# Performance work log

Hardware: AMD Instinct MI355X
Metric: run time of the kernel (lower is better)

The kernel has to match this reference:

```python
import jax, jax.numpy as jnp
import numpy as np

B, S, H = 4, 2048, 1024
NH = 1                     # source code only type-checks with 1 head (see notes)
DH = H // NH               # head dim == hidden size
DT = 32                    # distance_type
LN_EPS = 1e-12


def setup_inputs() -> dict:
    key = jax.random.key(0)
    ks = jax.random.split(key, 12)
    sd = 0.02
    hidden_states = jax.random.normal(ks[0], (B, S, H), dtype=jnp.float32)
    attention_mask = jnp.zeros((B, 1, 1, S), dtype=jnp.float32)
    word_word_relation = jax.random.randint(ks[1], (B, S, S), 0, DT, dtype=jnp.int64)
    dist_emb = sd * jax.random.normal(ks[2], (DT, H), dtype=jnp.float32)
    dist_emb = dist_emb.at[0].set(0.0)  # padding_idx=0
    return {
        "hidden_states": hidden_states,
        "attention_mask": attention_mask,
        "word_word_relation": word_word_relation,
        "Wq": sd * jax.random.normal(ks[3], (H, H), dtype=jnp.float32),
        "bq": jnp.zeros((H,), dtype=jnp.float32),
        "Wk": sd * jax.random.normal(ks[4], (H, H), dtype=jnp.float32),
        "bk": jnp.zeros((H,), dtype=jnp.float32),
        "Wv": sd * jax.random.normal(ks[5], (H, H), dtype=jnp.float32),
        "bv": jnp.zeros((H,), dtype=jnp.float32),
        "dist_emb": dist_emb,
        "Wo": sd * jax.random.normal(ks[6], (H, H), dtype=jnp.float32),
        "bo": jnp.zeros((H,), dtype=jnp.float32),
        "ln_g": jnp.ones((H,), dtype=jnp.float32),
        "ln_b": jnp.zeros((H,), dtype=jnp.float32),
    }


def _split_heads(x):
    # [B,S,H] -> [B,NH,S,DH]
    return x.reshape(B, S, NH, DH).transpose(0, 2, 1, 3)


def reference(hidden_states, attention_mask, word_word_relation, Wq, bq, Wk, bk,
              Wv, bv, dist_emb, Wo, bo, ln_g, ln_b):
    q = _split_heads(hidden_states @ Wq.T + bq)   # [B,NH,S,DH]
    k = _split_heads(hidden_states @ Wk.T + bk)
    v = _split_heads(hidden_states @ Wv.T + bv)

    # raw QK^T scores [B,NH,S,S]
    scores = jnp.einsum('bhqd,bhkd->bhqk', q, k)

    # query . distance_embedding^T : [B,NH,S,DT]
    word_dot_distance = jnp.einsum('bhqd,td->bhqt', q, dist_emb)

    rel = word_word_relation[:, None, :, :]       # [B,1,S,S]
    # gather per-pair distance score along the distance-type axis
    dist_att = jnp.take_along_axis(word_dot_distance, rel, axis=3)  # [B,NH,S,S]
    mask_out = (rel == 1).astype(scores.dtype)    # keep only relation==1 pairs
    dist_att = dist_att * mask_out

    scores = (scores + dist_att) / jnp.sqrt(jnp.asarray(DH, scores.dtype))
    scores = scores + attention_mask              # additive BERT mask
    probs = jax.nn.softmax(scores, axis=-1)       # dropout p=0 -> identity

    ctx = jnp.einsum('bhqk,bhkd->bhqd', probs, v) # [B,NH,S,DH]
    ctx = ctx.transpose(0, 2, 1, 3).reshape(B, S, H)

    # BertSelfOutput: dense -> residual -> LayerNorm
    attn_out = ctx @ Wo.T + bo
    x = attn_out + hidden_states
    mu = jnp.mean(x, axis=-1, keepdims=True)
    var = jnp.mean(jnp.square(x - mu), axis=-1, keepdims=True)
    out = (x - mu) * jax.lax.rsqrt(var + LN_EPS) * ln_g + ln_b
    return out
```

## Files before the change

### kernel.cpp

```cpp
#include <hip/hip_runtime.h>

#define BM 128
#define BN 128
#define BKH 32

typedef __bf16 bf16x8 __attribute__((ext_vector_type(8)));
typedef __bf16 bf16x4 __attribute__((ext_vector_type(4)));
typedef float f32x4 __attribute__((ext_vector_type(4)));
typedef __bf16 bf16_t;

__device__ __forceinline__ void gl_lds16(const void* g, void* l) {
    __builtin_amdgcn_global_load_lds(
        (const __attribute__((address_space(1))) void*)g,
        (__attribute__((address_space(3))) void*)l, 16, 0, 0);
}

__global__ __launch_bounds__(256)
void cvt_all_kernel(const float* __restrict__ hid,
                    const float* __restrict__ w0, const float* __restrict__ w1,
                    const float* __restrict__ w2, const float* __restrict__ w3,
                    bf16_t* __restrict__ hidb, bf16_t* __restrict__ wb)
{
    const int bid = blockIdx.x;
    const float* src;
    bf16_t* dst;
    size_t off;
    if (bid < 8192) {
        src = hid; dst = hidb; off = (size_t)bid * 1024;
    } else {
        const int i = (bid - 8192) >> 10;
        src = (i == 0) ? w0 : (i == 1) ? w1 : (i == 2) ? w2 : w3;
        dst = wb + (size_t)i * 1024 * 1024;
        off = (size_t)((bid - 8192) & 1023) * 1024;
    }
    const size_t idx = off + threadIdx.x * 4;
    const float4 v = *(const float4*)(src + idx);
    bf16x4 o;
    o[0] = (__bf16)v.x; o[1] = (__bf16)v.y;
    o[2] = (__bf16)v.z; o[3] = (__bf16)v.w;
    *(bf16x4*)(dst + idx) = o;
}

template <int MODE, int SWIZ>
__global__ __launch_bounds__(256)
void gemm_bt(const bf16_t* __restrict__ A, const bf16_t* __restrict__ Bw,
             const float* __restrict__ bias, const float* __restrict__ bias2,
             const float* __restrict__ bias3,
             bf16_t* __restrict__ C, bf16_t* __restrict__ C2,
             int M, int N, int K,
             long long sAz, long long sBz, long long sCz,
             const bf16_t* __restrict__ resid,
             int Sdim, int DHdim)
{
    const int bz = blockIdx.z;
    const float* bi = bias;
    if (MODE == 0) {
        Bw += (long long)bz * N * K;
        bi = (bz == 0) ? bias : (bz == 1 ? bias2 : bias3);
        if (bz < 2) C += (long long)bz * sCz;
    } else {
        A += (long long)bz * sAz;
        Bw += (long long)bz * sBz;
        C += (long long)bz * sCz;
    }

    int m0, n0;
    if (SWIZ) {
        const int num_n = N / BN;
        const int pid = blockIdx.x;
        const int group = 8 * num_n;
        const int g = pid / group;
        m0 = (g * 8 + (pid % 8)) * BM;
        n0 = ((pid % group) / 8) * BN;
    } else {
        m0 = blockIdx.y * BM;
        n0 = blockIdx.x * BN;
    }
    const int tid = threadIdx.x;
    const int w = tid >> 6;
    const int lane = tid & 63;
    const int wr = w >> 1;
    const int wc = w & 1;
    const int srow = lane >> 2;
    const int scol = (lane & 3) * 8;
    const int frow = lane & 15;
    const int fk = (lane >> 4) * 8;

    __shared__ bf16_t smem[4 * BM * BKH];
    bf16_t* A0 = smem;
    bf16_t* A1 = smem + BM * BKH;
    bf16_t* B0 = smem + 2 * BM * BKH;
    bf16_t* B1 = smem + 3 * BM * BKH;

    f32x4 acc[4][4];
#pragma unroll
    for (int i = 0; i < 4; ++i)
#pragma unroll
        for (int j = 0; j < 4; ++j) acc[i][j] = (f32x4)0.0f;

    for (int k0 = 0; k0 < K; k0 += 2 * BKH) {
#pragma unroll
        for (int i = 0; i < 2; ++i) {
            const int r = i * 64 + w * 16;
            const bf16_t* ga = A + (size_t)(m0 + r + srow) * K + (k0 + scol);
            const bf16_t* gb = Bw + (size_t)(n0 + r + srow) * K + (k0 + scol);
            gl_lds16(ga,        &A0[r * BKH]);
            gl_lds16(ga + BKH,  &A1[r * BKH]);
            gl_lds16(gb,        &B0[r * BKH]);
            gl_lds16(gb + BKH,  &B1[r * BKH]);
        }
        __syncthreads();
#pragma unroll
        for (int h = 0; h < 2; ++h) {
            const bf16_t* Ah = h ? A1 : A0;
            const bf16_t* Bh = h ? B1 : B0;
            bf16x8 af[4], bfv[4];
#pragma unroll
            for (int t = 0; t < 4; ++t) {
                af[t]  = *(const bf16x8*)&Ah[(wr * 64 + t * 16 + frow) * BKH + fk];
                bfv[t] = *(const bf16x8*)&Bh[(wc * 64 + t * 16 + frow) * BKH + fk];
            }
#pragma unroll
            for (int mt = 0; mt < 4; ++mt)
#pragma unroll
                for (int nt = 0; nt < 4; ++nt)
                    acc[mt][nt] = __builtin_amdgcn_mfma_f32_16x16x32_bf16(
                        af[mt], bfv[nt], acc[mt][nt], 0, 0, 0);
        }
        __syncthreads();
    }

    const int crow = (lane >> 4) * 4;
    const int ccol = lane & 15;

    if (MODE == 0 && bz == 2) {
#pragma unroll
        for (int mt = 0; mt < 4; ++mt) {
            const int mb = m0 + wr * 64 + mt * 16 + crow;
#pragma unroll
            for (int nt = 0; nt < 4; ++nt) {
                const int n = n0 + wc * 64 + nt * 16 + ccol;
                const float bv = bi[n];
                const int b = mb >> 11;
                const int s = mb & 2047;
                union { ushort4 u; bf16_t h[4]; } pk;
#pragma unroll
                for (int r = 0; r < 4; ++r) pk.h[r] = (__bf16)(acc[mt][nt][r] + bv);
                *(ushort4*)&C2[(size_t)b * DHdim * Sdim + (size_t)n * Sdim + s] = pk.u;
            }
        }
        return;
    }

    bf16_t* tw = smem + w * (16 * 72);
    const int r0 = lane >> 3;
    const int cseg = (lane & 7) * 8;

    float bv[4];
    if (MODE == 0 || MODE == 4) {
#pragma unroll
        for (int nt = 0; nt < 4; ++nt)
            bv[nt] = bi[n0 + wc * 64 + nt * 16 + ccol];
    }

#pragma unroll
    for (int mt = 0; mt < 4; ++mt) {
#pragma unroll
        for (int nt = 0; nt < 4; ++nt) {
            const float badd = (MODE == 0 || MODE == 4) ? bv[nt] : 0.0f;
#pragma unroll
            for (int r = 0; r < 4; ++r)
                tw[(crow + r) * 72 + nt * 16 + ccol] = (__bf16)(acc[mt][nt][r] + badd);
        }
        bf16x8 va = *(const bf16x8*)&tw[r0 * 72 + cseg];
        bf16x8 vb = *(const bf16x8*)&tw[(r0 + 8) * 72 + cseg];

        const int gm_a = m0 + wr * 64 + mt * 16 + r0;
        const int gm_b = gm_a + 8;
        const int gn = n0 + wc * 64 + cseg;

        if (MODE == 0 || MODE == 3) {
            *(bf16x8*)&C[(size_t)gm_a * N + gn] = va;
            *(bf16x8*)&C[(size_t)gm_b * N + gn] = vb;
        } else {
            const bf16x8 xa = *(const bf16x8*)&resid[(size_t)gm_a * N + gn];
            const bf16x8 xb = *(const bf16x8*)&resid[(size_t)gm_b * N + gn];
            bf16x8 oa, ob;
#pragma unroll
            for (int j = 0; j < 8; ++j) {
                oa[j] = (__bf16)((float)va[j] + (float)xa[j]);
                ob[j] = (__bf16)((float)vb[j] + (float)xb[j]);
            }
            *(bf16x8*)&C[(size_t)gm_a * N + gn] = oa;
            *(bf16x8*)&C[(size_t)gm_b * N + gn] = ob;
        }
    }
}

__global__ __launch_bounds__(256)
void softmax_kernel(bf16_t* __restrict__ sc, const int* __restrict__ rel,
                    const bf16_t* __restrict__ q, const float* __restrict__ de,
                    const float* __restrict__ mask)
{
    constexpr int S = 2048, H = 1024;
    const int row = blockIdx.x;
    const int b = row >> 11;
    const int tid = threadIdx.x;
    const int w = tid >> 6, lane = tid & 63;
    __shared__ float rd1[4], rmax[4], rsum[4];

    const bf16x4 q4 = *(const bf16x4*)(q + (size_t)row * H + tid * 4);
    const float4 e4 = *(const float4*)(de + H + tid * 4);
    float pd = (float)q4[0] * e4.x + (float)q4[1] * e4.y
             + (float)q4[2] * e4.z + (float)q4[3] * e4.w;
#pragma unroll
    for (int off = 32; off; off >>= 1) pd += __shfl_xor(pd, off, 64);
    if (lane == 0) rd1[w] = pd;
    __syncthreads();
    const float d1s = (rd1[0] + rd1[1] + rd1[2] + rd1[3]) * 0.03125f;

    bf16_t* p = sc + (size_t)row * S;
    const bf16x8 x = *(const bf16x8*)(p + tid * 8);
    const int4 rl0 = *(const int4*)&rel[(size_t)row * S + tid * 8];
    const int4 rl1 = *(const int4*)&rel[(size_t)row * S + tid * 8 + 4];
    const float4 mk0 = *(const float4*)&mask[(size_t)b * S + tid * 8];
    const float4 mk1 = *(const float4*)&mask[(size_t)b * S + tid * 8 + 4];
    const int rls[8] = {rl0.x, rl0.y, rl0.z, rl0.w, rl1.x, rl1.y, rl1.z, rl1.w};
    const float mks[8] = {mk0.x, mk0.y, mk0.z, mk0.w, mk1.x, mk1.y, mk1.z, mk1.w};
    float v[8];
    float mx = -1e30f;
#pragma unroll
    for (int j = 0; j < 8; ++j) {
        v[j] = (float)x[j] * 0.03125f + mks[j] + (rls[j] == 1 ? d1s : 0.0f);
        mx = fmaxf(mx, v[j]);
    }
#pragma unroll
    for (int off = 32; off; off >>= 1) mx = fmaxf(mx, __shfl_xor(mx, off, 64));
    if (lane == 0) rmax[w] = mx;
    __syncthreads();
    mx = fmaxf(fmaxf(rmax[0], rmax[1]), fmaxf(rmax[2], rmax[3]));
    float sum = 0.0f;
#pragma unroll
    for (int j = 0; j < 8; ++j) { v[j] = __expf(v[j] - mx); sum += v[j]; }
#pragma unroll
    for (int off = 32; off; off >>= 1) sum += __shfl_xor(sum, off, 64);
    if (lane == 0) rsum[w] = sum;
    __syncthreads();
    sum = rsum[0] + rsum[1] + rsum[2] + rsum[3];
    const float inv = 1.0f / sum;
    bf16x8 o;
#pragma unroll
    for (int j = 0; j < 8; ++j) o[j] = (__bf16)(v[j] * inv);
    *(bf16x8*)(p + tid * 8) = o;
}

__global__ __launch_bounds__(256)
void ln_kernel(const bf16_t* __restrict__ x, const float* __restrict__ gamma,
               const float* __restrict__ beta, float* __restrict__ out)
{
    const int H = 1024;
    const int tid = threadIdx.x;
    const int half = tid >> 7;
    const int t7 = tid & 127;
    const size_t row = (size_t)blockIdx.x * 2 + half;
    const int w = tid >> 6, lane = tid & 63;
    const bf16x8 xv = *(const bf16x8*)(x + row * H + t7 * 8);
    float v[8], s = 0.0f, s2 = 0.0f;
#pragma unroll
    for (int j = 0; j < 8; ++j) {
        v[j] = (float)xv[j];
        s += v[j]; s2 += v[j] * v[j];
    }
#pragma unroll
    for (int off = 32; off; off >>= 1) {
        s += __shfl_xor(s, off, 64);
        s2 += __shfl_xor(s2, off, 64);
    }
    __shared__ float rs[4], rs2[4];
    if (lane == 0) { rs[w] = s; rs2[w] = s2; }
    __syncthreads();
    s  = rs[half * 2] + rs[half * 2 + 1];
    s2 = rs2[half * 2] + rs2[half * 2 + 1];
    const float mu  = s * (1.0f / H);
    const float var = s2 * (1.0f / H) - mu * mu;
    const float inv = rsqrtf(var + 1e-12f);
    const int c = t7 * 8;
    float4 o0, o1;
    o0.x = (v[0] - mu) * inv * gamma[c + 0] + beta[c + 0];
    o0.y = (v[1] - mu) * inv * gamma[c + 1] + beta[c + 1];
    o0.z = (v[2] - mu) * inv * gamma[c + 2] + beta[c + 2];
    o0.w = (v[3] - mu) * inv * gamma[c + 3] + beta[c + 3];
    o1.x = (v[4] - mu) * inv * gamma[c + 4] + beta[c + 4];
    o1.y = (v[5] - mu) * inv * gamma[c + 5] + beta[c + 5];
    o1.z = (v[6] - mu) * inv * gamma[c + 6] + beta[c + 6];
    o1.w = (v[7] - mu) * inv * gamma[c + 7] + beta[c + 7];
    *(float4*)(out + row * H + c) = o0;
    *(float4*)(out + row * H + c + 4) = o1;
}

extern "C" void kernel_launch(void* const* d_in, const int* in_sizes, int n_in,
                              void* d_out, int out_size, void* d_ws, size_t ws_size,
                              hipStream_t stream)
{
    constexpr int B = 4, S = 2048, H = 1024;
    const float* hid = (const float*)d_in[0];
    const float* am  = (const float*)d_in[1];
    const int*   rel = (const int*)d_in[2];
    const float* Wq  = (const float*)d_in[3];
    const float* bq  = (const float*)d_in[4];
    const float* Wk  = (const float*)d_in[5];
    const float* bk  = (const float*)d_in[6];
    const float* Wv  = (const float*)d_in[7];
    const float* bv  = (const float*)d_in[8];
    const float* de  = (const float*)d_in[9];
    const float* Wo  = (const float*)d_in[10];
    const float* bo  = (const float*)d_in[11];
    const float* lng = (const float*)d_in[12];
    const float* lnb = (const float*)d_in[13];
    float* out = (float*)d_out;

    char* ws = (char*)d_ws;
    const int n_tok = B * S;
    const size_t MB = 1024 * 1024;
    bf16_t* hidb = (bf16_t*)(ws);
    bf16_t* Wqb  = (bf16_t*)(ws + 16 * MB);
    bf16_t* Wob  = (bf16_t*)(ws + 22 * MB);
    bf16_t* qb   = (bf16_t*)(ws + 24 * MB);
    bf16_t* kb   = (bf16_t*)(ws + 40 * MB);
    bf16_t* vT   = (bf16_t*)(ws + 56 * MB);
    bf16_t* ctx  = (bf16_t*)(ws + 72 * MB);
    bf16_t* sc   = (bf16_t*)(ws + 88 * MB);
    bf16_t* xb   = (bf16_t*)(ws + 88 * MB);

    const dim3 blk(256);
    cvt_all_kernel<<<dim3(8192 + 4 * 1024), blk, 0, stream>>>(
        hid, Wq, Wk, Wv, Wo, hidb, Wqb);

    gemm_bt<0, 1><<<dim3(64 * 8, 1, 3), blk, 0, stream>>>(
        hidb, Wqb, bq, bk, bv, qb, vT, n_tok, H, H,
        0, 0, (long long)n_tok * H,
        nullptr, S, H);
    gemm_bt<3, 1><<<dim3(16 * 16, 1, B), blk, 0, stream>>>(
        qb, kb, nullptr, nullptr, nullptr, sc, nullptr, S, S, H,
        (long long)S * H, (long long)S * H, (long long)S * S,
        nullptr, S, H);
    softmax_kernel<<<dim3(B * S), blk, 0, stream>>>(sc, rel, qb, de, am);
    gemm_bt<3, 0><<<dim3(H / BN, S / BM, B), blk, 0, stream>>>(
        sc, vT, nullptr, nullptr, nullptr, ctx, nullptr, S, H, S,
        (long long)S * S, (long long)H * S, (long long)S * H,
        nullptr, S, H);
    gemm_bt<4, 0><<<dim3(H / BN, n_tok / BM, 1), blk, 0, stream>>>(
        ctx, Wob, bo, nullptr, nullptr, xb, nullptr, n_tok, H, H, 0, 0, 0,
        hidb, S, H);
    ln_kernel<<<dim3(n_tok / 2), blk, 0, stream>>>(xb, lng, lnb, out);
}
```

Measured before the change: 386.2 us.

## Fuse softmax exp and distance bias into QK GEMM, defer normalization to PV

```diff
diff --git a/kernel.cpp b/kernel.cpp
--- a/kernel.cpp
+++ b/kernel.cpp
@@ -19,9 +19,15 @@
 void cvt_all_kernel(const float* __restrict__ hid,
                     const float* __restrict__ w0, const float* __restrict__ w1,
                     const float* __restrict__ w2, const float* __restrict__ w3,
-                    bf16_t* __restrict__ hidb, bf16_t* __restrict__ wb)
+                    bf16_t* __restrict__ hidb, bf16_t* __restrict__ wb,
+                    float* __restrict__ rowsum)
 {
     const int bid = blockIdx.x;
+    if (bid >= 12288) {
+        const int i = (bid - 12288) * 1024 + threadIdx.x * 4;
+        *(float4*)(rowsum + i) = make_float4(0.f, 0.f, 0.f, 0.f);
+        return;
+    }
     const float* src;
     bf16_t* dst;
     size_t off;
@@ -50,6 +56,8 @@
              int M, int N, int K,
              long long sAz, long long sBz, long long sCz,
              const bf16_t* __restrict__ resid,
+             const int* __restrict__ rel, const float* __restrict__ maskp,
+             const float* __restrict__ de1, float* __restrict__ rowsum,
              int Sdim, int DHdim)
 {
     const int bz = blockIdx.z;
@@ -91,12 +99,15 @@
     bf16_t* A1 = smem + BM * BKH;
     bf16_t* B0 = smem + 2 * BM * BKH;
     bf16_t* B1 = smem + 3 * BM * BKH;
+    float* d1f = (float*)(smem + 2 * BM * BKH);
 
     f32x4 acc[4][4];
 #pragma unroll
     for (int i = 0; i < 4; ++i)
 #pragma unroll
         for (int j = 0; j < 4; ++j) acc[i][j] = (f32x4)0.0f;
+
+    float d1acc[4] = {0.f, 0.f, 0.f, 0.f};
 
     for (int k0 = 0; k0 < K; k0 += 2 * BKH) {
 #pragma unroll
@@ -120,12 +131,37 @@
                 af[t]  = *(const bf16x8*)&Ah[(wr * 64 + t * 16 + frow) * BKH + fk];
                 bfv[t] = *(const bf16x8*)&Bh[(wc * 64 + t * 16 + frow) * BKH + fk];
             }
+            if (MODE == 5 && wc == 0) {
+                const float* dp = de1 + k0 + h * BKH + fk;
+                const float4 e0 = *(const float4*)dp;
+                const float4 e1 = *(const float4*)(dp + 4);
+#pragma unroll
+                for (int t = 0; t < 4; ++t) {
+                    d1acc[t] += (float)af[t][0] * e0.x + (float)af[t][1] * e0.y
+                              + (float)af[t][2] * e0.z + (float)af[t][3] * e0.w
+                              + (float)af[t][4] * e1.x + (float)af[t][5] * e1.y
+                              + (float)af[t][6] * e1.z + (float)af[t][7] * e1.w;
+                }
+            }
 #pragma unroll
             for (int mt = 0; mt < 4; ++mt)
 #pragma unroll
                 for (int nt = 0; nt < 4; ++nt)
                     acc[mt][nt] = __builtin_amdgcn_mfma_f32_16x16x32_bf16(
                         af[mt], bfv[nt], acc[mt][nt], 0, 0, 0);
+        }
+        __syncthreads();
+    }
+
+    if (MODE == 5) {
+        if (wc == 0) {
+#pragma unroll
+            for (int t = 0; t < 4; ++t) {
+                float s = d1acc[t];
+                s += __shfl_xor(s, 16, 64);
+                s += __shfl_xor(s, 32, 64);
+                if (lane < 16) d1f[wr * 64 + t * 16 + lane] = s;
+            }
         }
         __syncthreads();
     }
@@ -179,9 +215,56 @@
         const int gm_b = gm_a + 8;
         const int gn = n0 + wc * 64 + cseg;
 
-        if (MODE == 0 || MODE == 3) {
+        if (MODE == 0) {
             *(bf16x8*)&C[(size_t)gm_a * N + gn] = va;
             *(bf16x8*)&C[(size_t)gm_b * N + gn] = vb;
+        } else if (MODE == 5) {
+            const float da = d1f[wr * 64 + mt * 16 + r0];
+            const float db = d1f[wr * 64 + mt * 16 + r0 + 8];
+            const long long ra = ((long long)bz * M + gm_a) * N + gn;
+            const long long rb = ((long long)bz * M + gm_b) * N + gn;
+            const int4 ra0 = *(const int4*)&rel[ra];
+            const int4 ra1 = *(const int4*)&rel[ra + 4];
+            const int4 rb0 = *(const int4*)&rel[rb];
+            const int4 rb1 = *(const int4*)&rel[rb + 4];
+            const float4 mk0 = *(const float4*)&maskp[(size_t)bz * N + gn];
+            const float4 mk1 = *(const float4*)&maskp[(size_t)bz * N + gn + 4];
+            const int rlsa[8] = {ra0.x, ra0.y, ra0.z, ra0.w, ra1.x, ra1.y, ra1.z, ra1.w};
+            const int rlsb[8] = {rb0.x, rb0.y, rb0.z, rb0.w, rb1.x, rb1.y, rb1.z, rb1.w};
+            const float mks[8] = {mk0.x, mk0.y, mk0.z, mk0.w, mk1.x, mk1.y, mk1.z, mk1.w};
+            bf16x8 oa, ob;
+            float sa = 0.f, sb = 0.f;
+#pragma unroll
+            for (int j = 0; j < 8; ++j) {
+                const float ea = __expf(((float)va[j] + (rlsa[j] == 1 ? da : 0.f))
+                                        * 0.03125f + mks[j]);
+                const float eb = __expf(((float)vb[j] + (rlsb[j] == 1 ? db : 0.f))
+                                        * 0.03125f + mks[j]);
+                sa += ea; sb += eb;
+                oa[j] = (__bf16)ea; ob[j] = (__bf16)eb;
+            }
+#pragma unroll
+            for (int off = 4; off; off >>= 1) {
+                sa += __shfl_down(sa, off, 64);
+                sb += __shfl_down(sb, off, 64);
+            }
+            if ((lane & 7) == 0) {
+                atomicAdd(&rowsum[(size_t)bz * M + gm_a], sa);
+                atomicAdd(&rowsum[(size_t)bz * M + gm_b], sb);
+            }
+            *(bf16x8*)&C[(size_t)gm_a * N + gn] = oa;
+            *(bf16x8*)&C[(size_t)gm_b * N + gn] = ob;
+        } else if (MODE == 6) {
+            const float inva = 1.0f / rowsum[(size_t)bz * M + gm_a];
+            const float invb = 1.0f / rowsum[(size_t)bz * M + gm_b];
+            bf16x8 oa, ob;
+#pragma unroll
+            for (int j = 0; j < 8; ++j) {
+                oa[j] = (__bf16)((float)va[j] * inva);
+                ob[j] = (__bf16)((float)vb[j] * invb);
+            }
+            *(bf16x8*)&C[(size_t)gm_a * N + gn] = oa;
+            *(bf16x8*)&C[(size_t)gm_b * N + gn] = ob;
         } else {
             const bf16x8 xa = *(const bf16x8*)&resid[(size_t)gm_a * N + gn];
             const bf16x8 xb = *(const bf16x8*)&resid[(size_t)gm_b * N + gn];
@@ -195,63 +278,6 @@
             *(bf16x8*)&C[(size_t)gm_b * N + gn] = ob;
         }
     }
-}
-
-__global__ __launch_bounds__(256)
-void softmax_kernel(bf16_t* __restrict__ sc, const int* __restrict__ rel,
-                    const bf16_t* __restrict__ q, const float* __restrict__ de,
-                    const float* __restrict__ mask)
-{
-    constexpr int S = 2048, H = 1024;
-    const int row = blockIdx.x;
-    const int b = row >> 11;
-    const int tid = threadIdx.x;
-    const int w = tid >> 6, lane = tid & 63;
-    __shared__ float rd1[4], rmax[4], rsum[4];
-
-    const bf16x4 q4 = *(const bf16x4*)(q + (size_t)row * H + tid * 4);
-    const float4 e4 = *(const float4*)(de + H + tid * 4);
-    float pd = (float)q4[0] * e4.x + (float)q4[1] * e4.y
-             + (float)q4[2] * e4.z + (float)q4[3] * e4.w;
-#pragma unroll
-    for (int off = 32; off; off >>= 1) pd += __shfl_xor(pd, off, 64);
-    if (lane == 0) rd1[w] = pd;
-    __syncthreads();
-    const float d1s = (rd1[0] + rd1[1] + rd1[2] + rd1[3]) * 0.03125f;
-
-    bf16_t* p = sc + (size_t)row * S;
-    const bf16x8 x = *(const bf16x8*)(p + tid * 8);
-    const int4 rl0 = *(const int4*)&rel[(size_t)row * S + tid * 8];
-    const int4 rl1 = *(const int4*)&rel[(size_t)row * S + tid * 8 + 4];
-    const float4 mk0 = *(const float4*)&mask[(size_t)b * S + tid * 8];
-    const float4 mk1 = *(const float4*)&mask[(size_t)b * S + tid * 8 + 4];
-    const int rls[8] = {rl0.x, rl0.y, rl0.z, rl0.w, rl1.x, rl1.y, rl1.z, rl1.w};
-    const float mks[8] = {mk0.x, mk0.y, mk0.z, mk0.w, mk1.x, mk1.y, mk1.z, mk1.w};
-    float v[8];
-    float mx = -1e30f;
-#pragma unroll
-    for (int j = 0; j < 8; ++j) {
-        v[j] = (float)x[j] * 0.03125f + mks[j] + (rls[j] == 1 ? d1s : 0.0f);
-        mx = fmaxf(mx, v[j]);
-    }
-#pragma unroll
-    for (int off = 32; off; off >>= 1) mx = fmaxf(mx, __shfl_xor(mx, off, 64));
-    if (lane == 0) rmax[w] = mx;
-    __syncthreads();
-    mx = fmaxf(fmaxf(rmax[0], rmax[1]), fmaxf(rmax[2], rmax[3]));
-    float sum = 0.0f;
-#pragma unroll
-    for (int j = 0; j < 8; ++j) { v[j] = __expf(v[j] - mx); sum += v[j]; }
-#pragma unroll
-    for (int off = 32; off; off >>= 1) sum += __shfl_xor(sum, off, 64);
-    if (lane == 0) rsum[w] = sum;
-    __syncthreads();
-    sum = rsum[0] + rsum[1] + rsum[2] + rsum[3];
-    const float inv = 1.0f / sum;
-    bf16x8 o;
-#pragma unroll
-    for (int j = 0; j < 8; ++j) o[j] = (__bf16)(v[j] * inv);
-    *(bf16x8*)(p + tid * 8) = o;
 }
 
 __global__ __launch_bounds__(256)
@@ -331,26 +357,26 @@
     bf16_t* ctx  = (bf16_t*)(ws + 72 * MB);
     bf16_t* sc   = (bf16_t*)(ws + 88 * MB);
     bf16_t* xb   = (bf16_t*)(ws + 88 * MB);
+    float*  rowsum = (float*)(ws + 120 * MB);
 
     const dim3 blk(256);
-    cvt_all_kernel<<<dim3(8192 + 4 * 1024), blk, 0, stream>>>(
-        hid, Wq, Wk, Wv, Wo, hidb, Wqb);
+    cvt_all_kernel<<<dim3(8192 + 4 * 1024 + 8), blk, 0, stream>>>(
+        hid, Wq, Wk, Wv, Wo, hidb, Wqb, rowsum);
 
     gemm_bt<0, 1><<<dim3(64 * 8, 1, 3), blk, 0, stream>>>(
         hidb, Wqb, bq, bk, bv, qb, vT, n_tok, H, H,
         0, 0, (long long)n_tok * H,
-        nullptr, S, H);
-    gemm_bt<3, 1><<<dim3(16 * 16, 1, B), blk, 0, stream>>>(
+        nullptr, nullptr, nullptr, nullptr, nullptr, S, H);
+    gemm_bt<5, 1><<<dim3(16 * 16, 1, B), blk, 0, stream>>>(
         qb, kb, nullptr, nullptr, nullptr, sc, nullptr, S, S, H,
         (long long)S * H, (long long)S * H, (long long)S * S,
-        nullptr, S, H);
-    softmax_kernel<<<dim3(B * S), blk, 0, stream>>>(sc, rel, qb, de, am);
-    gemm_bt<3, 0><<<dim3(H / BN, S / BM, B), blk, 0, stream>>>(
+        nullptr, rel, am, de + H, rowsum, S, H);
+    gemm_bt<6, 0><<<dim3(H / BN, S / BM, B), blk, 0, stream>>>(
         sc, vT, nullptr, nullptr, nullptr, ctx, nullptr, S, H, S,
         (long long)S * S, (long long)H * S, (long long)S * H,
-        nullptr, S, H);
+        nullptr, nullptr, nullptr, nullptr, rowsum, S, H);
     gemm_bt<4, 0><<<dim3(H / BN, n_tok / BM, 1), blk, 0, stream>>>(
         ctx, Wob, bo, nullptr, nullptr, xb, nullptr, n_tok, H, H, 0, 0, 0,
-        hidb, S, H);
+        hidb, nullptr, nullptr, nullptr, nullptr, S, H);
     ln_kernel<<<dim3(n_tok / 2), blk, 0, stream>>>(xb, lng, lnb, out);
 }
```

Result: no change. 381.5 us (-1.2%).
